# Performance work log

Hardware: AMD Instinct MI355X
Metric: run time of the kernel (lower is better)

## Reference

```python
import jax, jax.numpy as jnp
import numpy as np

COORD_DIM, PARAM_DIM, H, L, O = 3, 8, 128, 5, 5
B, N_PTS = 16, 50000


def setup_inputs() -> dict:
    key = jax.random.key(0)
    ks = jax.random.split(key, 16)
    def w(k, shape, fan_in):
        return jax.random.normal(k, shape, dtype=jnp.float32) / np.sqrt(fan_in)
    inp = {
        "coords": jax.random.normal(ks[0], (B, N_PTS, COORD_DIM), dtype=jnp.float32),
        "params": jax.random.normal(ks[1], (B, PARAM_DIM), dtype=jnp.float32),
        # branch MLP: param_dim -> H (x5 hidden, rowdy tanh) -> H*O
        "branch_W0": w(ks[2], (PARAM_DIM, H), PARAM_DIM),
        "branch_b0": jnp.zeros((H,), jnp.float32),
        "branch_Wh": w(ks[3], (L - 1, H, H), H),
        "branch_bh": jnp.zeros((L - 1, H), jnp.float32),
        "branch_alpha": jnp.ones((L, H), jnp.float32),
        "branch_Wf": w(ks[4], (H, H * O), H),
        "branch_bf": jnp.zeros((H * O,), jnp.float32),
        # trunk: coord_dim -> H (x5, FiLM by branch cumsum, rowdy tanh) -> H
        "trunk_W0": w(ks[5], (COORD_DIM, H), COORD_DIM),
        "trunk_b0": jnp.zeros((H,), jnp.float32),
        "trunk_Wh": w(ks[6], (L - 1, H, H), H),
        "trunk_bh": jnp.zeros((L - 1, H), jnp.float32),
        "trunk_alpha": jnp.ones((L, H), jnp.float32),
        "trunk_Wf": w(ks[7], (H, H), H),
        "trunk_bf": jnp.zeros((H,), jnp.float32),
    }
    return inp


def reference(coords, params, branch_W0, branch_b0, branch_Wh, branch_bh,
              branch_alpha, branch_Wf, branch_bf, trunk_W0, trunk_b0,
              trunk_Wh, trunk_bh, trunk_alpha, trunk_Wf, trunk_bf):
    # ---- branch MLP with RowdyActivation, keeping hidden outputs ----
    h = branch_alpha[0] * jnp.tanh(params @ branch_W0 + branch_b0)  # (B,H)
    hiddens = [h]
    for i in range(L - 1):
        h = branch_alpha[i + 1] * jnp.tanh(h @ branch_Wh[i] + branch_bh[i])
        hiddens.append(h)
    branch_out = h @ branch_Wf + branch_bf  # (B, H*O)
    # cumulative sums S_i = sum_{j<=i} hidden_j
    S = [hiddens[0]]
    for i in range(1, L):
        S.append(hiddens[i] + S[-1])
    # ---- trunk with FiLM modulation ----
    x = coords @ trunk_W0 + trunk_b0                       # (B,n,H)
    x = trunk_alpha[0] * jnp.tanh(x * S[0][:, None, :])
    for i in range(1, L):
        x = x @ trunk_Wh[i - 1] + trunk_bh[i - 1]
        x = trunk_alpha[i] * jnp.tanh(x * S[i][:, None, :])
    YL = x @ trunk_Wf + trunk_bf                           # (B,n,H)
    ZL = branch_out.reshape(B, O, H)                       # (B,O,H)
    # out[b,n,o] = sum_h ZL[b,o,h] * YL[b,n,h]  (tiled matmul, no (B,n,O,H) temp)
    return jnp.einsum('bnh,boh->bno', YL, ZL)
```

## Files before the change

### kernel.cpp

```cpp
#include <hip/hip_runtime.h>
#include <math.h>

#define H      128
#define LNUM   5
#define ONUM   5
#define BATCH  16
#define NPTS   50000
#define TP     128
#define XROW   152

#define K2LOG2E 2.8853900817779268f

typedef _Float16      half8    __attribute__((ext_vector_type(8)));
typedef float         floatx4  __attribute__((ext_vector_type(4)));
typedef unsigned int  uint2v   __attribute__((ext_vector_type(2)));
typedef unsigned int  uint4v   __attribute__((ext_vector_type(4)));
typedef unsigned short ushort8_t __attribute__((ext_vector_type(8)));

static __device__ __forceinline__ unsigned short f2h(float f) {
    _Float16 h = (_Float16)f;
    return __builtin_bit_cast(unsigned short, h);
}
static __device__ __forceinline__ unsigned int packh(float a, float b) {
    return (unsigned int)f2h(a) | ((unsigned int)f2h(b) << 16);
}

__global__ __launch_bounds__(512)
void fold_kernel(const float* __restrict__ params,
                 const float* __restrict__ bW0, const float* __restrict__ bb0,
                 const float* __restrict__ bWh, const float* __restrict__ bbh,
                 const float* __restrict__ balpha,
                 const float* __restrict__ bWf, const float* __restrict__ bbf,
                 const float* __restrict__ tW0, const float* __restrict__ tb0,
                 const float* __restrict__ tWh, const float* __restrict__ tbh,
                 const float* __restrict__ tWf, const float* __restrict__ talpha,
                 const float* __restrict__ tbf,
                 unsigned short* __restrict__ w0s, unsigned short* __restrict__ whs,
                 unsigned short* __restrict__ wcomb, float* __restrict__ bcomb,
                 float* __restrict__ binit) {
    const int b = blockIdx.x, l = blockIdx.y, t = threadIdx.x;
    __shared__ float hbuf[H];
    __shared__ float Sneed[H];
    __shared__ float pbuf[8];
    __shared__ float zl_sh[ONUM][H];
    if (t < 8) pbuf[t] = params[b * 8 + t];
    __syncthreads();

    float scum = 0.0f;
    if (t < H) {
        float acc = bb0[t];
        for (int k = 0; k < 8; ++k) acc += pbuf[k] * bW0[k * H + t];
        float h = balpha[t] * tanhf(acc);
        hbuf[t] = h;
        scum = h;
        if (l == 0) Sneed[t] = scum;
    }
    for (int i = 1; i < LNUM; ++i) {
        __syncthreads();
        float hn = 0.0f;
        if (t < H) {
            const float* Wl = bWh + (i - 1) * H * H;
            float a2 = bbh[(i - 1) * H + t];
            for (int k = 0; k < H; ++k) a2 += hbuf[k] * Wl[k * H + t];
            hn = balpha[i * H + t] * tanhf(a2);
        }
        __syncthreads();
        if (t < H) {
            hbuf[t] = hn;
            scum += hn;
            if (i == l) Sneed[t] = scum;
        }
    }
    __syncthreads();

    if (l == 5) {
        for (int idx = t; idx < ONUM * H; idx += 512) {
            int o = idx >> 7, hh = idx & 127;
            float z = bbf[o * H + hh];
            for (int k = 0; k < H; ++k) z += hbuf[k] * bWf[k * (H * ONUM) + o * H + hh];
            zl_sh[o][hh] = z;
        }
        __syncthreads();
        for (int j = t; j < 16 * H; j += 512) {
            int o = j >> 7, f = j & 127;
            float v = 0.0f;
            if (o < ONUM) {
                const float* wfr = tWf + f * H;
                float s = 0.0f;
                for (int h = 0; h < H; ++h) s += wfr[h] * zl_sh[o][h];
                v = talpha[4 * H + f] * s;
            }
            wcomb[b * 16 * H + j] = f2h(v);
        }
        if (t < 16) {
            float v = 0.0f;
            if (t < ONUM)
                for (int h = 0; h < H; ++h) v += tbf[h] * zl_sh[t][h];
            bcomb[b * 16 + t] = v;
        }
    } else if (l == 0) {
        if (t < H) binit[(b * LNUM + 0) * H + t] = K2LOG2E * Sneed[t] * tb0[t];
        unsigned int* dst = (unsigned int*)(w0s + b * H * 32);
        for (int j = t; j < H * 16; j += 512) {
            int f = j >> 4, k0 = (j & 15) << 1;
            float s = K2LOG2E * Sneed[f];
            float v0 = (k0 < 3)     ? s * tW0[k0 * H + f]       : 0.0f;
            float v1 = (k0 + 1 < 3) ? s * tW0[(k0 + 1) * H + f] : 0.0f;
            dst[j] = packh(v0, v1);
        }
    } else {
        if (t < H) binit[(b * LNUM + l) * H + t] = K2LOG2E * Sneed[t] * tbh[(l - 1) * H + t];
        const float* Wsrc = tWh + (l - 1) * H * H;
        unsigned int* dst = (unsigned int*)(whs + (b * 4 + (l - 1)) * H * H);
        for (int j = t; j < H * H / 2; j += 512) {
            int f = j >> 6, k0 = (j & 63) << 1;
            float s = K2LOG2E * Sneed[f];
            dst[j] = packh(s * Wsrc[k0 * H + f] * talpha[(l - 1) * H + k0],
                           s * Wsrc[(k0 + 1) * H + f] * talpha[(l - 1) * H + k0 + 1]);
        }
    }
}

__global__ __launch_bounds__(256, 3)
void trunk_kernel(const float* __restrict__ coords,
                  const unsigned short* __restrict__ w0s,
                  const unsigned short* __restrict__ whs,
                  const float* __restrict__ binit,
                  const unsigned short* __restrict__ wcomb,
                  const float* __restrict__ bcomb,
                  float* __restrict__ out) {
    const int b    = blockIdx.y;
    const int n0   = blockIdx.x * TP;
    const int tid  = threadIdx.x;
    const int lane = tid & 63;
    const int w    = tid >> 6;
    const int q    = lane >> 4;
    const int c    = lane & 15;
    const int mq   = w * 32;

    __shared__ unsigned short xs[TP * XROW];

    int valid = NPTS - n0; if (valid > TP) valid = TP;
    {
        int p = tid >> 1, hh = tid & 1;
        if (hh == 0) {
            float c0 = 0.f, c1 = 0.f, c2 = 0.f;
            if (p < valid) {
                const float* cp = coords + ((size_t)b * NPTS + n0 + p) * 3;
                c0 = cp[0]; c1 = cp[1]; c2 = cp[2];
            }
            uint4v z;
            z.x = __builtin_bit_cast(unsigned int, __builtin_amdgcn_cvt_pkrtz(c0, c1));
            z.y = __builtin_bit_cast(unsigned int, __builtin_amdgcn_cvt_pkrtz(c2, 0.0f));
            z.z = 0; z.w = 0;
            *(uint4v*)&xs[p * XROW + 0] = z;
            uint4v zz = {0, 0, 0, 0};
            *(uint4v*)&xs[p * XROW + 8] = zz;
        } else {
            uint4v zz = {0, 0, 0, 0};
            *(uint4v*)&xs[p * XROW + 16] = zz;
            *(uint4v*)&xs[p * XROW + 24] = zz;
        }
    }
    __syncthreads();

    floatx4 acc[2][8];

    {
        const unsigned short* w0b = w0s + b * H * 32;
        const float* bi0 = &binit[(b * LNUM + 0) * H];
        half8 af[2];
        floatx4 bi4[2];
        #pragma unroll
        for (int mt = 0; mt < 2; ++mt) {
            af[mt] = __builtin_bit_cast(half8,
                *(const ushort8_t*)&w0b[(mq + mt * 16 + c) * 32 + q * 8]);
            bi4[mt] = *(const floatx4*)&bi0[mq + mt * 16 + q * 4];
        }
        __builtin_amdgcn_s_setprio(1);
        #pragma unroll
        for (int nt = 0; nt < 8; ++nt) {
            half8 bfr = __builtin_bit_cast(half8,
                *(const ushort8_t*)&xs[(nt * 16 + c) * XROW + q * 8]);
            #pragma unroll
            for (int mt = 0; mt < 2; ++mt)
                acc[mt][nt] = __builtin_amdgcn_mfma_f32_16x16x32_f16(af[mt], bfr, bi4[mt], 0, 0, 0);
        }
        __builtin_amdgcn_s_setprio(0);
    }
    __syncthreads();
    #pragma unroll
    for (int mt = 0; mt < 2; ++mt) {
        int f0 = mq + mt * 16 + q * 4;
        #pragma unroll
        for (int nt = 0; nt < 8; ++nt) {
            int pt = nt * 16 + c;
            floatx4 v = acc[mt][nt];
            #pragma unroll
            for (int r = 0; r < 4; ++r) {
                float e  = __builtin_amdgcn_exp2f(v[r]);
                float rc = __builtin_amdgcn_rcpf(e + 1.0f);
                v[r] = __builtin_fmaf(-2.0f, rc, 1.0f);
            }
            uint2v u;
            u.x = __builtin_bit_cast(unsigned int, __builtin_amdgcn_cvt_pkrtz(v[0], v[1]));
            u.y = __builtin_bit_cast(unsigned int, __builtin_amdgcn_cvt_pkrtz(v[2], v[3]));
            *(uint2v*)&xs[pt * XROW + f0] = u;
        }
    }

    for (int l = 1; l <= 4; ++l) {
        const unsigned short* wl = whs + (b * 4 + (l - 1)) * H * H;
        const float* bi = &binit[(b * LNUM + l) * H];
        floatx4 bi4[2];
        #pragma unroll
        for (int mt = 0; mt < 2; ++mt)
            bi4[mt] = *(const floatx4*)&bi[mq + mt * 16 + q * 4];
        __syncthreads();
        __builtin_amdgcn_s_setprio(1);
        #pragma unroll
        for (int s = 0; s < 4; ++s) {
            half8 af[2];
            #pragma unroll
            for (int mt = 0; mt < 2; ++mt)
                af[mt] = __builtin_bit_cast(half8,
                    *(const ushort8_t*)&wl[(mq + mt * 16 + c) * H + s * 32 + q * 8]);
            #pragma unroll
            for (int nt = 0; nt < 8; ++nt) {
                half8 bfr = __builtin_bit_cast(half8,
                    *(const ushort8_t*)&xs[(nt * 16 + c) * XROW + s * 32 + q * 8]);
                if (s == 0) {
                    #pragma unroll
                    for (int mt = 0; mt < 2; ++mt)
                        acc[mt][nt] = __builtin_amdgcn_mfma_f32_16x16x32_f16(af[mt], bfr, bi4[mt], 0, 0, 0);
                } else {
                    #pragma unroll
                    for (int mt = 0; mt < 2; ++mt)
                        acc[mt][nt] = __builtin_amdgcn_mfma_f32_16x16x32_f16(af[mt], bfr, acc[mt][nt], 0, 0, 0);
                }
            }
        }
        __builtin_amdgcn_s_setprio(0);
        __syncthreads();
        #pragma unroll
        for (int mt = 0; mt < 2; ++mt) {
            int f0 = mq + mt * 16 + q * 4;
            #pragma unroll
            for (int nt = 0; nt < 8; ++nt) {
                int pt = nt * 16 + c;
                floatx4 v = acc[mt][nt];
                #pragma unroll
                for (int r = 0; r < 4; ++r) {
                    float e  = __builtin_amdgcn_exp2f(v[r]);
                    float rc = __builtin_amdgcn_rcpf(e + 1.0f);
                    v[r] = __builtin_fmaf(-2.0f, rc, 1.0f);
                }
                uint2v u;
                u.x = __builtin_bit_cast(unsigned int, __builtin_amdgcn_cvt_pkrtz(v[0], v[1]));
                u.y = __builtin_bit_cast(unsigned int, __builtin_amdgcn_cvt_pkrtz(v[2], v[3]));
                *(uint2v*)&xs[pt * XROW + f0] = u;
            }
        }
    }
    __syncthreads();

    {
        floatx4 bc = *(const floatx4*)&bcomb[b * 16 + q * 4];
        floatx4 oacc[2];
        const unsigned short* wc = wcomb + b * 16 * H;
        #pragma unroll
        for (int s = 0; s < 4; ++s) {
            half8 af = __builtin_bit_cast(half8,
                *(const ushort8_t*)&wc[c * H + s * 32 + q * 8]);
            #pragma unroll
            for (int nt = 0; nt < 2; ++nt) {
                half8 bfr = __builtin_bit_cast(half8,
                    *(const ushort8_t*)&xs[(w * 32 + nt * 16 + c) * XROW + s * 32 + q * 8]);
                if (s == 0)
                    oacc[nt] = __builtin_amdgcn_mfma_f32_16x16x32_f16(af, bfr, bc, 0, 0, 0);
                else
                    oacc[nt] = __builtin_amdgcn_mfma_f32_16x16x32_f16(af, bfr, oacc[nt], 0, 0, 0);
            }
        }
        #pragma unroll
        for (int nt = 0; nt < 2; ++nt) {
            int pt = n0 + w * 32 + nt * 16 + c;
            if (pt < NPTS) {
                float* op = out + ((size_t)b * NPTS + pt) * ONUM;
                if (q == 0) {
                    op[0] = oacc[nt][0]; op[1] = oacc[nt][1];
                    op[2] = oacc[nt][2]; op[3] = oacc[nt][3];
                } else if (q == 1) {
                    op[4] = oacc[nt][0];
                }
            }
        }
    }
}

extern "C" void kernel_launch(void* const* d_in, const int* in_sizes, int n_in,
                              void* d_out, int out_size, void* d_ws, size_t ws_size,
                              hipStream_t stream) {
    const float* coords       = (const float*)d_in[0];
    const float* params       = (const float*)d_in[1];
    const float* branch_W0    = (const float*)d_in[2];
    const float* branch_b0    = (const float*)d_in[3];
    const float* branch_Wh    = (const float*)d_in[4];
    const float* branch_bh    = (const float*)d_in[5];
    const float* branch_alpha = (const float*)d_in[6];
    const float* branch_Wf    = (const float*)d_in[7];
    const float* branch_bf    = (const float*)d_in[8];
    const float* trunk_W0     = (const float*)d_in[9];
    const float* trunk_b0     = (const float*)d_in[10];
    const float* trunk_Wh     = (const float*)d_in[11];
    const float* trunk_bh     = (const float*)d_in[12];
    const float* trunk_alpha  = (const float*)d_in[13];
    const float* trunk_Wf     = (const float*)d_in[14];
    const float* trunk_bf     = (const float*)d_in[15];
    float* out = (float*)d_out;

    char* ws = (char*)d_ws;
    float*          binit = (float*)(ws + 0);
    unsigned short* wcomb = (unsigned short*)(ws + 40960);
    float*          bcomb = (float*)(ws + 106496);
    unsigned short* w0s   = (unsigned short*)(ws + 107520);
    unsigned short* whs   = (unsigned short*)(ws + 238592);

    fold_kernel<<<dim3(BATCH, 6), 512, 0, stream>>>(params, branch_W0, branch_b0,
                                                    branch_Wh, branch_bh, branch_alpha,
                                                    branch_Wf, branch_bf,
                                                    trunk_W0, trunk_b0, trunk_Wh, trunk_bh,
                                                    trunk_Wf, trunk_alpha, trunk_bf,
                                                    w0s, whs, wcomb, bcomb, binit);
    trunk_kernel<<<dim3((NPTS + TP - 1) / TP, BATCH), 256, 0, stream>>>(
        coords, w0s, whs, binit, wcomb, bcomb, out);
}
```

Measured before the change: 290.9 us.

## Double-buffer trunk activations in LDS to halve per-layer barriers

Activations now ping-pong between two LDS buffers, so each layer reads one buffer and writes its tanh output to the other, with a single __syncthreads per layer instead of two. The row pitch shrinks from 152 to 136 halves to fit both buffers, and the launch bound drops from 3 to 2 blocks per CU. The tanh epilogue is regrouped into pairs of floats so the compiler can emit packed math. Doubling LDS and lowering the occupancy hint may cut latency hiding, and the new row pitch may change LDS bank conflicts.

```diff
diff --git a/kernel.cpp b/kernel.cpp
--- a/kernel.cpp
+++ b/kernel.cpp
@@ -7,12 +7,13 @@
 #define BATCH  16
 #define NPTS   50000
 #define TP     128
-#define XROW   152
+#define XROW   136
 
 #define K2LOG2E 2.8853900817779268f
 
 typedef _Float16      half8    __attribute__((ext_vector_type(8)));
 typedef float         floatx4  __attribute__((ext_vector_type(4)));
+typedef float         floatx2  __attribute__((ext_vector_type(2)));
 typedef unsigned int  uint2v   __attribute__((ext_vector_type(2)));
 typedef unsigned int  uint4v   __attribute__((ext_vector_type(4)));
 typedef unsigned short ushort8_t __attribute__((ext_vector_type(8)));
@@ -121,7 +122,7 @@
     }
 }
 
-__global__ __launch_bounds__(256, 3)
+__global__ __launch_bounds__(256, 2)
 void trunk_kernel(const float* __restrict__ coords,
                   const unsigned short* __restrict__ w0s,
                   const unsigned short* __restrict__ whs,
@@ -138,7 +139,7 @@
     const int c    = lane & 15;
     const int mq   = w * 32;
 
-    __shared__ unsigned short xs[TP * XROW];
+    __shared__ unsigned short xs[2][TP * XROW];
 
     int valid = NPTS - n0; if (valid > TP) valid = TP;
     {
@@ -153,18 +154,49 @@
             z.x = __builtin_bit_cast(unsigned int, __builtin_amdgcn_cvt_pkrtz(c0, c1));
             z.y = __builtin_bit_cast(unsigned int, __builtin_amdgcn_cvt_pkrtz(c2, 0.0f));
             z.z = 0; z.w = 0;
-            *(uint4v*)&xs[p * XROW + 0] = z;
+            *(uint4v*)&xs[0][p * XROW + 0] = z;
             uint4v zz = {0, 0, 0, 0};
-            *(uint4v*)&xs[p * XROW + 8] = zz;
+            *(uint4v*)&xs[0][p * XROW + 8] = zz;
         } else {
             uint4v zz = {0, 0, 0, 0};
-            *(uint4v*)&xs[p * XROW + 16] = zz;
-            *(uint4v*)&xs[p * XROW + 24] = zz;
+            *(uint4v*)&xs[0][p * XROW + 16] = zz;
+            *(uint4v*)&xs[0][p * XROW + 24] = zz;
         }
     }
     __syncthreads();
 
     floatx4 acc[2][8];
+
+    auto tanh2 = [](floatx2 x) -> floatx2 {
+        floatx2 e;
+        e[0] = __builtin_amdgcn_exp2f(x[0]);
+        e[1] = __builtin_amdgcn_exp2f(x[1]);
+        floatx2 d = e + 1.0f;
+        floatx2 rc;
+        rc[0] = __builtin_amdgcn_rcpf(d[0]);
+        rc[1] = __builtin_amdgcn_rcpf(d[1]);
+        floatx2 m2 = {-2.0f, -2.0f}, one = {1.0f, 1.0f};
+        return __builtin_elementwise_fma(m2, rc, one);
+    };
+
+    auto epi = [&](unsigned short* dst) {
+        #pragma unroll
+        for (int mt = 0; mt < 2; ++mt) {
+            int f0 = mq + mt * 16 + q * 4;
+            #pragma unroll
+            for (int nt = 0; nt < 8; ++nt) {
+                int pt = nt * 16 + c;
+                floatx4 v = acc[mt][nt];
+                floatx2 lo = {v[0], v[1]}, hi = {v[2], v[3]};
+                lo = tanh2(lo);
+                hi = tanh2(hi);
+                uint2v u;
+                u.x = __builtin_bit_cast(unsigned int, __builtin_amdgcn_cvt_pkrtz(lo[0], lo[1]));
+                u.y = __builtin_bit_cast(unsigned int, __builtin_amdgcn_cvt_pkrtz(hi[0], hi[1]));
+                *(uint2v*)&dst[pt * XROW + f0] = u;
+            }
+        }
+    };
 
     {
         const unsigned short* w0b = w0s + b * H * 32;
@@ -181,42 +213,25 @@
         #pragma unroll
         for (int nt = 0; nt < 8; ++nt) {
             half8 bfr = __builtin_bit_cast(half8,
-                *(const ushort8_t*)&xs[(nt * 16 + c) * XROW + q * 8]);
+                *(const ushort8_t*)&xs[0][(nt * 16 + c) * XROW + q * 8]);
             #pragma unroll
             for (int mt = 0; mt < 2; ++mt)
                 acc[mt][nt] = __builtin_amdgcn_mfma_f32_16x16x32_f16(af[mt], bfr, bi4[mt], 0, 0, 0);
         }
         __builtin_amdgcn_s_setprio(0);
     }
+    epi(&xs[1][0]);
     __syncthreads();
-    #pragma unroll
-    for (int mt = 0; mt < 2; ++mt) {
-        int f0 = mq + mt * 16 + q * 4;
-        #pragma unroll
-        for (int nt = 0; nt < 8; ++nt) {
-            int pt = nt * 16 + c;
-            floatx4 v = acc[mt][nt];
-            #pragma unroll
-            for (int r = 0; r < 4; ++r) {
-                float e  = __builtin_amdgcn_exp2f(v[r]);
-                float rc = __builtin_amdgcn_rcpf(e + 1.0f);
-                v[r] = __builtin_fmaf(-2.0f, rc, 1.0f);
-            }
-            uint2v u;
-            u.x = __builtin_bit_cast(unsigned int, __builtin_amdgcn_cvt_pkrtz(v[0], v[1]));
-            u.y = __builtin_bit_cast(unsigned int, __builtin_amdgcn_cvt_pkrtz(v[2], v[3]));
-            *(uint2v*)&xs[pt * XROW + f0] = u;
-        }
-    }
 
     for (int l = 1; l <= 4; ++l) {
+        const int rb = l & 1;
         const unsigned short* wl = whs + (b * 4 + (l - 1)) * H * H;
         const float* bi = &binit[(b * LNUM + l) * H];
         floatx4 bi4[2];
         #pragma unroll
         for (int mt = 0; mt < 2; ++mt)
             bi4[mt] = *(const floatx4*)&bi[mq + mt * 16 + q * 4];
-        __syncthreads();
+        const unsigned short* src = &xs[rb][0];
         __builtin_amdgcn_s_setprio(1);
         #pragma unroll
         for (int s = 0; s < 4; ++s) {
@@ -228,7 +243,7 @@
             #pragma unroll
             for (int nt = 0; nt < 8; ++nt) {
                 half8 bfr = __builtin_bit_cast(half8,
-                    *(const ushort8_t*)&xs[(nt * 16 + c) * XROW + s * 32 + q * 8]);
+                    *(const ushort8_t*)&src[(nt * 16 + c) * XROW + s * 32 + q * 8]);
                 if (s == 0) {
                     #pragma unroll
                     for (int mt = 0; mt < 2; ++mt)
@@ -241,28 +256,9 @@
             }
         }
         __builtin_amdgcn_s_setprio(0);
+        epi(&xs[1 - rb][0]);
         __syncthreads();
-        #pragma unroll
-        for (int mt = 0; mt < 2; ++mt) {
-            int f0 = mq + mt * 16 + q * 4;
-            #pragma unroll
-            for (int nt = 0; nt < 8; ++nt) {
-                int pt = nt * 16 + c;
-                floatx4 v = acc[mt][nt];
-                #pragma unroll
-                for (int r = 0; r < 4; ++r) {
-                    float e  = __builtin_amdgcn_exp2f(v[r]);
-                    float rc = __builtin_amdgcn_rcpf(e + 1.0f);
-                    v[r] = __builtin_fmaf(-2.0f, rc, 1.0f);
-                }
-                uint2v u;
-                u.x = __builtin_bit_cast(unsigned int, __builtin_amdgcn_cvt_pkrtz(v[0], v[1]));
-                u.y = __builtin_bit_cast(unsigned int, __builtin_amdgcn_cvt_pkrtz(v[2], v[3]));
-                *(uint2v*)&xs[pt * XROW + f0] = u;
-            }
-        }
-    }
-    __syncthreads();
+    }
 
     {
         floatx4 bc = *(const floatx4*)&bcomb[b * 16 + q * 4];
@@ -275,7 +271,7 @@
             #pragma unroll
             for (int nt = 0; nt < 2; ++nt) {
                 half8 bfr = __builtin_bit_cast(half8,
-                    *(const ushort8_t*)&xs[(w * 32 + nt * 16 + c) * XROW + s * 32 + q * 8]);
+                    *(const ushort8_t*)&xs[1][(w * 32 + nt * 16 + c) * XROW + s * 32 + q * 8]);
                 if (s == 0)
                     oacc[nt] = __builtin_amdgcn_mfma_f32_16x16x32_f16(af, bfr, bc, 0, 0, 0);
                 else
```

Measured after the change: 314.7 us. 1.08x slower.
